# Performance work log

Hardware: AMD Instinct MI355X
Metric: run time of the kernel (lower is better)

The kernel has to match this reference:

```python
import jax, jax.numpy as jnp
import numpy as np

OUT_CH = 4096
IN_FEAT = 11008
BIT = 4
BIT_BOUND = BIT + 2  # bit + 2
EPS = 1e-05


def _round_ste(x):
    # straight-through round: identity gradient
    return x + jax.lax.stop_gradient(jnp.round(x) - x)


def fake_quant(w, scale, bit):
    """u_quant_w_func_alpha_linear_channelwise_div forward:
    per-out-channel uniform symmetric quantization with learnable bit.
    w: [O, I], scale: [O, 1], bit: [O, 1]
    """
    bit_r = _round_ste(bit)
    # quant_max = max(2^(b-1)-1, 1); quant_min = min(-(2^(b-1)-1), -1) = -quant_max
    qmax = jnp.maximum(jnp.exp2(bit_r - 1.0) - 1.0, 1.0)
    qmin = -qmax
    scale = jnp.maximum(scale, EPS)
    w_int = jnp.clip(_round_ste(w / scale), qmin, qmax)
    return w_int * scale


def setup_inputs() -> dict:
    key = jax.random.key(0)
    k_w, k_a = jax.random.split(key)
    weight = jax.random.normal(k_w, (OUT_CH, IN_FEAT), dtype=jnp.float32) * 0.02
    # alh = |N(mean=0.1, std=0.1)| per constructor
    alh = jnp.abs(0.1 + 0.1 * jax.random.normal(k_a, (OUT_CH, 1), dtype=jnp.float32))
    bit = jnp.full((OUT_CH, 1), float(BIT), dtype=jnp.float32)
    return {"weight": weight, "alh": alh, "bit": bit, "init_weight_bit": BIT}


def reference(weight, alh, bit, init_weight_bit):
    # bit = clamp(|bit|, 1, bit_bound).detach() + bit - bit.detach()  (STE clamp)
    bit_eff = (jax.lax.stop_gradient(jnp.clip(jnp.abs(bit), 1.0, float(BIT_BOUND)))
               + bit - jax.lax.stop_gradient(bit))
    # Training-time scale_renew is a no-op at init (old_bit == round(bit)),
    # so forward reduces to the STE fake-quantizer on the weight.
    return fake_quant(weight, alh, bit_eff)
```

## Files before the change

### kernel.cpp

```cpp
#include <hip/hip_runtime.h>
#include <hip/hip_bf16.h>

#define OUT_CH 4096
#define IN_FEAT 11008
#define NVEC (IN_FEAT / 4)
#define EPS 1e-5f
#define BIT_BOUND 6.0f

typedef float fvec4 __attribute__((ext_vector_type(4)));

__global__ __launch_bounds__(256) void fake_quant_kernel(
    const float* __restrict__ weight,
    const float* __restrict__ alh,
    const float* __restrict__ bit,
    float* __restrict__ out)
{
    const int row = blockIdx.x;
    const int tid = threadIdx.x;

    const fvec4* __restrict__ wrow =
        (const fvec4*)(weight + (size_t)row * IN_FEAT);
    fvec4* __restrict__ orow = (fvec4*)(out + (size_t)row * IN_FEAT);

    fvec4 w[10];
    #pragma unroll
    for (int j = 0; j < 10; ++j)
        w[j] = __builtin_nontemporal_load(&wrow[tid + j * 256]);

    const float s = fmaxf(alh[row], EPS);
    const float b_eff = fminf(fmaxf(fabsf(bit[row]), 1.0f), BIT_BOUND);
    const float b_r = rintf(b_eff);
    const float qmax = fmaxf(exp2f(b_r - 1.0f) - 1.0f, 1.0f);
    const float qmin = -qmax;

    auto q4 = [&](fvec4 v) -> fvec4 {
        fvec4 r;
        r.x = fminf(fmaxf(rintf(v.x / s), qmin), qmax) * s;
        r.y = fminf(fmaxf(rintf(v.y / s), qmin), qmax) * s;
        r.z = fminf(fmaxf(rintf(v.z / s), qmin), qmax) * s;
        r.w = fminf(fmaxf(rintf(v.w / s), qmin), qmax) * s;
        return r;
    };

    #pragma unroll
    for (int j = 0; j < 10; ++j)
        __builtin_nontemporal_store(q4(w[j]), &orow[tid + j * 256]);

    if (tid < (NVEC - 2560)) {
        fvec4 wt = __builtin_nontemporal_load(&wrow[tid + 2560]);
        __builtin_nontemporal_store(q4(wt), &orow[tid + 2560]);
    }
}

extern "C" void kernel_launch(void* const* d_in, const int* in_sizes, int n_in,
                              void* d_out, int out_size, void* d_ws, size_t ws_size,
                              hipStream_t stream) {
    const float* weight = (const float*)d_in[0];
    const float* alh    = (const float*)d_in[1];
    const float* bit    = (const float*)d_in[2];
    float* out = (float*)d_out;

    fake_quant_kernel<<<OUT_CH, 256, 0, stream>>>(weight, alh, bit, out);
}
```

Before: 295.0 us.

## Process two rows per block with a rolling seven-deep load/store pipeline

Each block now handles two consecutive rows, so there are half as many blocks, and it streams the combined 5504 vectors through a 7-entry register ring. Each slot's next load is issued right after its store, instead of loading 10 vectors up front and then storing them all. The goal is to keep memory requests in flight steadily and remove the poorly used tail iteration in each row. The cost is per-element selection of scale and qmax plus fewer, longer blocks, which may reduce the parallelism available to hide latency.

```diff
diff --git a/kernel.cpp b/kernel.cpp
--- a/kernel.cpp
+++ b/kernel.cpp
@@ -4,6 +4,10 @@
 #define OUT_CH 4096
 #define IN_FEAT 11008
 #define NVEC (IN_FEAT / 4)
+#define PAIRVEC (2 * NVEC)
+#define NB 21
+#define TAILN (PAIRVEC - NB * 256)
+#define DEPTH 7
 #define EPS 1e-5f
 #define BIT_BOUND 6.0f
 
@@ -15,25 +19,28 @@
     const float* __restrict__ bit,
     float* __restrict__ out)
 {
-    const int row = blockIdx.x;
+    const int pair = blockIdx.x;
+    const int r0 = 2 * pair;
     const int tid = threadIdx.x;
 
     const fvec4* __restrict__ wrow =
-        (const fvec4*)(weight + (size_t)row * IN_FEAT);
-    fvec4* __restrict__ orow = (fvec4*)(out + (size_t)row * IN_FEAT);
+        (const fvec4*)(weight + (size_t)r0 * IN_FEAT);
+    fvec4* __restrict__ orow = (fvec4*)(out + (size_t)r0 * IN_FEAT);
 
-    fvec4 w[10];
+    fvec4 w[DEPTH];
     #pragma unroll
-    for (int j = 0; j < 10; ++j)
+    for (int j = 0; j < DEPTH; ++j)
         w[j] = __builtin_nontemporal_load(&wrow[tid + j * 256]);
 
-    const float s = fmaxf(alh[row], EPS);
-    const float b_eff = fminf(fmaxf(fabsf(bit[row]), 1.0f), BIT_BOUND);
-    const float b_r = rintf(b_eff);
-    const float qmax = fmaxf(exp2f(b_r - 1.0f) - 1.0f, 1.0f);
-    const float qmin = -qmax;
+    const float s0 = fmaxf(alh[r0], EPS);
+    const float s1 = fmaxf(alh[r0 + 1], EPS);
+    const float be0 = fminf(fmaxf(fabsf(bit[r0]), 1.0f), BIT_BOUND);
+    const float be1 = fminf(fmaxf(fabsf(bit[r0 + 1]), 1.0f), BIT_BOUND);
+    const float qm0 = fmaxf(exp2f(rintf(be0) - 1.0f) - 1.0f, 1.0f);
+    const float qm1 = fmaxf(exp2f(rintf(be1) - 1.0f) - 1.0f, 1.0f);
 
-    auto q4 = [&](fvec4 v) -> fvec4 {
+    auto q4 = [](fvec4 v, float s, float qmax) -> fvec4 {
+        const float qmin = -qmax;
         fvec4 r;
         r.x = fminf(fmaxf(rintf(v.x / s), qmin), qmax) * s;
         r.y = fminf(fmaxf(rintf(v.y / s), qmin), qmax) * s;
@@ -42,13 +49,27 @@
         return r;
     };
 
+    #pragma unroll 7
+    for (int k = 0; k < NB - DEPTH; ++k) {
+        const int vidx = tid + k * 256;
+        const bool in_r1 = vidx >= NVEC;
+        const float s = in_r1 ? s1 : s0;
+        const float qm = in_r1 ? qm1 : qm0;
+        __builtin_nontemporal_store(q4(w[k % DEPTH], s, qm), &orow[vidx]);
+        w[k % DEPTH] = __builtin_nontemporal_load(&wrow[vidx + DEPTH * 256]);
+    }
     #pragma unroll
-    for (int j = 0; j < 10; ++j)
-        __builtin_nontemporal_store(q4(w[j]), &orow[tid + j * 256]);
-
-    if (tid < (NVEC - 2560)) {
-        fvec4 wt = __builtin_nontemporal_load(&wrow[tid + 2560]);
-        __builtin_nontemporal_store(q4(wt), &orow[tid + 2560]);
+    for (int k = NB - DEPTH; k < NB; ++k) {
+        const int vidx = tid + k * 256;
+        const bool in_r1 = vidx >= NVEC;
+        const float s = in_r1 ? s1 : s0;
+        const float qm = in_r1 ? qm1 : qm0;
+        __builtin_nontemporal_store(q4(w[k % DEPTH], s, qm), &orow[vidx]);
+    }
+    if (tid < TAILN) {
+        const int vidx = NB * 256 + tid;
+        fvec4 v = __builtin_nontemporal_load(&wrow[vidx]);
+        __builtin_nontemporal_store(q4(v, s1, qm1), &orow[vidx]);
     }
 }
 
@@ -60,5 +81,5 @@
     const float* bit    = (const float*)d_in[2];
     float* out = (float*)d_out;
 
-    fake_quant_kernel<<<OUT_CH, 256, 0, stream>>>(weight, alh, bit, out);
+    fake_quant_kernel<<<OUT_CH / 2, 256, 0, stream>>>(weight, alh, bit, out);
 }
```

Result: slower. 304.8 us (+3.3%).
